# Kernel optimization log

Hardware: AMD Instinct MI355X
Metric: run time of the kernel (lower is better)

The kernel has to match this reference:

```python
import jax, jax.numpy as jnp
import numpy as np

G = 32        # group_num
PD = 8        # primary capsule dim
OC = 10       # output caps (classes)
OD = 16       # output dim
GS = 36       # group_size = primary spatial 6*6
N_ITERS = 3   # routing iterations


def conv2d(x, w, stride):
    return jax.lax.conv_general_dilated(
        x, w, window_strides=(stride, stride), padding='VALID',
        dimension_numbers=('NCHW', 'OIHW', 'NCHW'))


def squash(x):
    l2 = jnp.sum(x * x, axis=-1, keepdims=True)
    l = jnp.sqrt(l2)
    return x * (l2 / (1.0 + l2)) / (l + 1e-8)


def setup_inputs() -> dict:
    key = jax.random.key(0)
    ks = jax.random.split(key, 6)
    B = 256
    inp = jax.random.normal(ks[0], (B, 1, 28, 28), dtype=jnp.float32)
    W1 = jax.random.normal(ks[1], (256, 1, 9, 9), dtype=jnp.float32) * 0.05
    b1 = jnp.zeros((256,), dtype=jnp.float32)
    W2 = jax.random.normal(ks[2], (G * PD, 256, 9, 9), dtype=jnp.float32) * 0.01
    b2 = jnp.zeros((G * PD,), dtype=jnp.float32)
    Wcaps = jax.random.normal(ks[3], (G, GS, PD, OC * OD), dtype=jnp.float32) * 0.01
    b_route = jnp.zeros((G, 1, GS, OC), dtype=jnp.float32)
    return {'input': inp, 'W1': W1, 'b1': b1, 'W2': W2, 'b2': b2,
            'Wcaps': Wcaps, 'b_route': b_route}


def reference(input, W1, b1, W2, b2, Wcaps, b_route):
    B = input.shape[0]
    # conv1 + relu: (B,256,20,20)
    x = jax.nn.relu(conv2d(input, W1, 1) + b1[None, :, None, None])
    # primary caps conv: (B,256,6,6)
    y = conv2d(x, W2, 2) + b2[None, :, None, None]
    H = y.shape[2]
    # (B,G,PD,H,W) -> (B,G,H,W,PD) -> (B,G,GS,PD)
    y = y.reshape(B, G, PD, H, H).transpose(0, 1, 3, 4, 2).reshape(B, G, GS, PD)
    u = squash(y)
    # capsule predictions: (B,G,GS,OC,OD)
    up = jnp.einsum('bgsi,gsio->bgso', u, Wcaps).reshape(B, G, GS, OC, OD)
    # routing logits: (B,G,GS,OC)
    b = jnp.broadcast_to(jnp.transpose(b_route, (1, 0, 2, 3)), (B, G, GS, OC))
    v = None
    for r in range(N_ITERS):
        c = jax.nn.softmax(b, axis=3)                       # (B,G,GS,OC)
        s = jnp.einsum('bgso,bgsod->bgod', c, up)           # (B,G,OC,OD)
        v = squash(s)
        if r < N_ITERS - 1:
            b = b + jnp.einsum('bgsod,bgod->bgso', up, v)
    v = v.sum(axis=1)                                       # (B,OC,OD)
    probs = jnp.sqrt(jnp.sum(v * v, axis=2))                # (B,OC)
    return v, probs
```

## Files before the change

kernel.cpp:

```cpp
#include <hip/hip_runtime.h>
#include <math.h>


typedef float floatx4 __attribute__((ext_vector_type(4)));
typedef __bf16 bf16x8 __attribute__((ext_vector_type(8)));
typedef unsigned uintx4 __attribute__((ext_vector_type(4)));

#define XHI_OFF 0u
#define XLO_OFF 58720256u
#define WHI_OFF 117440512u
#define WLO_OFF 128974848u
#define Y2_OFF  140509184u
#define VP_OFF  0u
#define Y2_BYTES 9437184u

#define SL_IY   88
#define SL_IMG  1760
#define SL_PAR  7072
#define SL_STRIDE 14336

#define TAPSTRIDE 65536

__device__ __forceinline__ void bf16split(float v, short& hs, short& ls) {
  unsigned u = __builtin_bit_cast(unsigned, v);
  unsigned r = (u + 0x7FFFu + ((u >> 16) & 1u)) & 0xFFFF0000u;
  hs = (short)(r >> 16);
  float lo = v - __builtin_bit_cast(float, r);
  unsigned u2 = __builtin_bit_cast(unsigned, lo);
  unsigned r2 = u2 + 0x7FFFu + ((u2 >> 16) & 1u);
  ls = (short)(r2 >> 16);
}

__device__ __forceinline__ void stage7(const short* gp, short* lp) {
#pragma unroll
  for (int c = 0; c < 7; c++)
    __builtin_amdgcn_global_load_lds(
        (const __attribute__((address_space(1))) void*)(gp + c * 512),
        (__attribute__((address_space(3))) void*)(lp + c * 512), 16, 0, 0);
}

__global__ __launch_bounds__(320) void conv1_k(
    const float* __restrict__ inp, const float* __restrict__ W1,
    const float* __restrict__ b1, short* __restrict__ xhi,
    short* __restrict__ xlo) {
  __shared__ __align__(16) float img[784];
  __shared__ float wl[81 * 34];
  const int blk = blockIdx.x;
  const int b = blk >> 3;
  const int cbase = (blk & 7) * 32;
  const int t = threadIdx.x;

  const float4* src = (const float4*)(inp + b * 784);
  for (int idx = t; idx < 196; idx += 320) ((float4*)img)[idx] = src[idx];
  for (int idx = t; idx < 2592; idx += 320) {
    int c = idx / 81, tap = idx - c * 81;
    wl[tap * 34 + c] = W1[(cbase + c) * 81 + tap];
  }
  __syncthreads();

  const int oy = t >> 4;
  const int ct = t & 15;
  const int c0 = cbase + ct * 2;
  const float bias0 = b1[c0], bias1 = b1[c0 + 1];
  float acc0[20], acc1[20];
#pragma unroll
  for (int ox = 0; ox < 20; ox++) { acc0[ox] = bias0; acc1[ox] = bias1; }

#pragma unroll 1
  for (int i = 0; i < 9; i++) {
    float wr0[9], wr1[9];
#pragma unroll
    for (int j = 0; j < 9; j++) {
      float2 wv = *(const float2*)&wl[(i * 9 + j) * 34 + ct * 2];
      wr0[j] = wv.x; wr1[j] = wv.y;
    }
    float xr[28];
    const float4* rp = (const float4*)&img[(oy + i) * 28];
#pragma unroll
    for (int k = 0; k < 7; k++) {
      float4 v = rp[k];
      xr[4 * k] = v.x; xr[4 * k + 1] = v.y; xr[4 * k + 2] = v.z; xr[4 * k + 3] = v.w;
    }
#pragma unroll
    for (int j = 0; j < 9; j++)
#pragma unroll
      for (int ox = 0; ox < 20; ox++) {
        acc0[ox] = fmaf(xr[ox + j], wr0[j], acc0[ox]);
        acc1[ox] = fmaf(xr[ox + j], wr1[j], acc1[ox]);
      }
  }

  const int icgG = c0 >> 3;
  const long sbase = ((long)(icgG * 64 + (b >> 2))) * SL_STRIDE
                   + (long)(b & 3) * SL_IMG + (long)oy * SL_IY + (c0 & 7);
#pragma unroll
  for (int ox = 0; ox < 20; ox++) {
    float v0 = fmaxf(acc0[ox], 0.f), v1 = fmaxf(acc1[ox], 0.f);
    short h0, l0, h1, l1;
    bf16split(v0, h0, l0);
    bf16split(v1, h1, l1);
    long a = sbase + (ox & 1) * SL_PAR + (ox >> 1) * 8;
    *(short2*)&xhi[a] = make_short2(h0, h1);
    *(short2*)&xlo[a] = make_short2(l0, l1);
  }
  {
    long a0 = sbase + 80;
    *(short2*)&xhi[a0] = make_short2(0, 0);
    *(short2*)&xlo[a0] = make_short2(0, 0);
    long a1 = sbase + SL_PAR + 80;
    *(short2*)&xhi[a1] = make_short2(0, 0);
    *(short2*)&xlo[a1] = make_short2(0, 0);
  }
}

__global__ __launch_bounds__(256) void wtrans_k(
    const float* __restrict__ W2, short* __restrict__ whi,
    short* __restrict__ wlo) {
  __shared__ short lh[81 * 258];
  __shared__ short ll[81 * 258];
  const int blk = blockIdx.x;
  const int icg = blk & 31, ocg = blk >> 5;
  const int t = threadIdx.x;

  for (int idx = t; idx < 20736; idx += 256) {
    int c = idx / 648, r = idx - c * 648;
    int ics = r / 81, tap = r - ics * 81;
    float v = W2[(long)(ocg * 32 + c) * 20736 + icg * 648 + r];
    short h, l;
    bf16split(v, h, l);
    lh[tap * 258 + c * 8 + ics] = h;
    ll[tap * 258 + c * 8 + ics] = l;
  }
  __syncthreads();
  const long obase = (long)icg * 2048 + ocg * 256 + t;
#pragma unroll 1
  for (int tap = 0; tap < 88; tap++) {
    short h = 0, l = 0;
    if (tap < 81) { h = lh[tap * 258 + t]; l = ll[tap * 258 + t]; }
    whi[obase + (long)tap * TAPSTRIDE] = h;
    wlo[obase + (long)tap * TAPSTRIDE] = l;
  }
}

__global__ __launch_bounds__(256, 2) void conv2_k(
    const short* __restrict__ xhi, const short* __restrict__ xlo,
    const short* __restrict__ whi, const short* __restrict__ wlo,
    float* __restrict__ y2) {
  __shared__ __align__(16) short slab[2][SL_STRIDE];

  const int blk = blockIdx.x;
  const int ks = blk & 7;
  const int mb = blk >> 3;
  const int t = threadIdx.x;
  const int lane = t & 63;
  const int q = lane >> 4;
  const int ln16 = lane & 15;
  const int wv = t >> 6;

  int combo[9];
#pragma unroll
  for (int mt = 0; mt < 9; mt++) {
    int row = mt * 16 + ln16;
    int im = row / 36;
    int pos = row - im * 36;
    int oy = pos / 6, ox = pos - oy * 6;
    combo[mt] = im * SL_IMG + oy * (2 * SL_IY) + ox * 8;
  }

  floatx4 acc[9][4];
#pragma unroll
  for (int mt = 0; mt < 9; mt++)
#pragma unroll
    for (int nt = 0; nt < 4; nt++) acc[mt][nt] = (floatx4)0.f;

  const int stoff = wv * 7 * 512 + lane * 8;

  stage7(xhi + (long)(ks * 4 * 64 + mb) * SL_STRIDE + stoff, &slab[0][stoff]);

#pragma unroll 1
  for (int icg = 0; icg < 4; icg++) {
    const int icgG = ks * 4 + icg;
    const long wb0 = ((long)icgG * 256 + wv * 64 + ln16) * 8 + (long)q * TAPSTRIDE;

    __syncthreads();
    stage7(xlo + (long)(icgG * 64 + mb) * SL_STRIDE + stoff, &slab[1][stoff]);

    {
      bf16x8 cbh[4];
#pragma unroll
      for (int nt = 0; nt < 4; nt++) cbh[nt] = *(const bf16x8*)&whi[wb0 + nt * 128];
#pragma unroll 1
      for (int kst = 0; kst < 21; kst++) {
        const int t0n = (kst < 20) ? (kst + 1) * 4 : 80;
        bf16x8 nbh[4], cbl[4];
#pragma unroll
        for (int nt = 0; nt < 4; nt++) {
          nbh[nt] = *(const bf16x8*)&whi[wb0 + (long)t0n * TAPSTRIDE + nt * 128];
          cbl[nt] = *(const bf16x8*)&wlo[wb0 + (long)(kst * 4) * TAPSTRIDE + nt * 128];
        }
        const int tap = kst * 4 + q;
        const int i = tap / 9, j = tap - i * 9;
        const int aoff = (j & 1) * SL_PAR + i * SL_IY + (j >> 1) * 8;
#pragma unroll
        for (int bb = 0; bb < 3; bb++) {
          bf16x8 av[3];
#pragma unroll
          for (int m3 = 0; m3 < 3; m3++)
            av[m3] = *(const bf16x8*)&slab[0][aoff + combo[bb * 3 + m3]];
#pragma unroll
          for (int nt = 0; nt < 4; nt++)
#pragma unroll
            for (int m3 = 0; m3 < 3; m3++)
              acc[bb * 3 + m3][nt] = __builtin_amdgcn_mfma_f32_16x16x32_bf16(
                  av[m3], cbh[nt], acc[bb * 3 + m3][nt], 0, 0, 0);
#pragma unroll
          for (int nt = 0; nt < 4; nt++)
#pragma unroll
            for (int m3 = 0; m3 < 3; m3++)
              acc[bb * 3 + m3][nt] = __builtin_amdgcn_mfma_f32_16x16x32_bf16(
                  av[m3], cbl[nt], acc[bb * 3 + m3][nt], 0, 0, 0);
        }
#pragma unroll
        for (int nt = 0; nt < 4; nt++) cbh[nt] = nbh[nt];
      }
    }

    __syncthreads();
    if (icg < 3)
      stage7(xhi + (long)((icgG + 1) * 64 + mb) * SL_STRIDE + stoff, &slab[0][stoff]);

    {
      bf16x8 cbh[4];
#pragma unroll
      for (int nt = 0; nt < 4; nt++) cbh[nt] = *(const bf16x8*)&whi[wb0 + nt * 128];
#pragma unroll 1
      for (int kst = 0; kst < 21; kst++) {
        const int t0n = (kst < 20) ? (kst + 1) * 4 : 80;
        bf16x8 nbh[4];
#pragma unroll
        for (int nt = 0; nt < 4; nt++)
          nbh[nt] = *(const bf16x8*)&whi[wb0 + (long)t0n * TAPSTRIDE + nt * 128];
        const int tap = kst * 4 + q;
        const int i = tap / 9, j = tap - i * 9;
        const int aoff = (j & 1) * SL_PAR + i * SL_IY + (j >> 1) * 8;
#pragma unroll
        for (int bb = 0; bb < 3; bb++) {
          bf16x8 av[3];
#pragma unroll
          for (int m3 = 0; m3 < 3; m3++)
            av[m3] = *(const bf16x8*)&slab[1][aoff + combo[bb * 3 + m3]];
#pragma unroll
          for (int nt = 0; nt < 4; nt++)
#pragma unroll
            for (int m3 = 0; m3 < 3; m3++)
              acc[bb * 3 + m3][nt] = __builtin_amdgcn_mfma_f32_16x16x32_bf16(
                  av[m3], cbh[nt], acc[bb * 3 + m3][nt], 0, 0, 0);
        }
#pragma unroll
        for (int nt = 0; nt < 4; nt++) cbh[nt] = nbh[nt];
      }
    }
  }

#pragma unroll
  for (int mt = 0; mt < 9; mt++)
#pragma unroll
    for (int nt = 0; nt < 4; nt++) {
      int oc = wv * 64 + nt * 16 + ln16;
      int rowb = mb * 144 + mt * 16 + q * 4;
#pragma unroll
      for (int r = 0; r < 4; r++)
        atomicAdd(&y2[(long)(rowb + r) * 256 + oc], acc[mt][nt][r]);
    }
}

__global__ __launch_bounds__(256) void caps_k(
    const float* __restrict__ y2, const float* __restrict__ b2,
    const float* __restrict__ Wcaps, const float* __restrict__ b_route,
    float* __restrict__ vpart) {
  __shared__ float u[288];
  __shared__ float usc[36];
  __shared__ float up[5760];
  __shared__ float bl[360];
  __shared__ float cl[360];
  __shared__ float sv[160];
  __shared__ float vv[160];
  __shared__ float scale[10];
  const int blk = blockIdx.x;
  const int g = blk & 31, b = blk >> 5;
  const int t = threadIdx.x;

  for (int idx = t; idx < 288; idx += 256) {
    int s = idx >> 3, d = idx & 7;
    u[idx] = y2[((long)b * 36 + s) * 256 + g * 8 + d] + b2[g * 8 + d];
  }
  for (int idx = t; idx < 360; idx += 256) bl[idx] = b_route[g * 360 + idx];
  __syncthreads();
  if (t < 36) {
    float l2 = 0.f;
#pragma unroll
    for (int d = 0; d < 8; d++) { float v = u[t * 8 + d]; l2 = fmaf(v, v, l2); }
    float l = sqrtf(l2);
    usc[t] = (l2 / (1.f + l2)) / (l + 1e-8f);
  }
  __syncthreads();
  for (int idx = t; idx < 288; idx += 256) u[idx] *= usc[idx >> 3];
  __syncthreads();
  for (int idx = t; idx < 5760; idx += 256) {
    int s = idx / 160, k = idx - s * 160;
    const float* wp = Wcaps + (g * 36 + s) * 8 * 160 + k;
    float a = 0.f;
#pragma unroll
    for (int d = 0; d < 8; d++) a = fmaf(u[s * 8 + d], wp[d * 160], a);
    up[idx] = a;
  }
  __syncthreads();

  for (int r = 0; r < 3; r++) {
    if (t < 36) {
      float m = bl[t * 10];
#pragma unroll
      for (int oc = 1; oc < 10; oc++) m = fmaxf(m, bl[t * 10 + oc]);
      float e[10]; float sum = 0.f;
#pragma unroll
      for (int oc = 0; oc < 10; oc++) { e[oc] = expf(bl[t * 10 + oc] - m); sum += e[oc]; }
      float inv = 1.f / sum;
#pragma unroll
      for (int oc = 0; oc < 10; oc++) cl[t * 10 + oc] = e[oc] * inv;
    }
    __syncthreads();
    if (t < 160) {
      const int oc = t >> 4;
      float a = 0.f;
#pragma unroll 1
      for (int s = 0; s < 36; s++) a = fmaf(cl[s * 10 + oc], up[s * 160 + t], a);
      sv[t] = a;
    }
    __syncthreads();
    if (t < 10) {
      float l2 = 0.f;
#pragma unroll
      for (int od = 0; od < 16; od++) { float v = sv[t * 16 + od]; l2 = fmaf(v, v, l2); }
      scale[t] = (l2 / (1.f + l2)) / (sqrtf(l2) + 1e-8f);
    }
    __syncthreads();
    if (t < 160) vv[t] = sv[t] * scale[t >> 4];
    __syncthreads();
    if (r < 2) {
      for (int idx = t; idx < 360; idx += 256) {
        int s = idx / 10, oc = idx - s * 10;
        float a = 0.f;
#pragma unroll
        for (int od = 0; od < 16; od++)
          a = fmaf(up[s * 160 + oc * 16 + od], vv[oc * 16 + od], a);
        bl[idx] += a;
      }
      __syncthreads();
    }
  }
  if (t < 160) vpart[(b * 32 + g) * 160 + t] = vv[t];
}

__global__ __launch_bounds__(192) void final_k(
    const float* __restrict__ vpart, float* __restrict__ out) {
  __shared__ float v[160];
  const int b = blockIdx.x, t = threadIdx.x;
  if (t < 160) {
    float a = 0.f;
#pragma unroll 4
    for (int g = 0; g < 32; g++) a += vpart[(b * 32 + g) * 160 + t];
    v[t] = a;
    out[b * 160 + t] = a;
  }
  __syncthreads();
  if (t < 10) {
    float l2 = 0.f;
#pragma unroll
    for (int od = 0; od < 16; od++) { float x = v[t * 16 + od]; l2 = fmaf(x, x, l2); }
    out[40960 + b * 10 + t] = sqrtf(l2);
  }
}

extern "C" void kernel_launch(void* const* d_in, const int* in_sizes, int n_in,
                              void* d_out, int out_size, void* d_ws, size_t ws_size,
                              hipStream_t stream) {
  const float* inp     = (const float*)d_in[0];
  const float* W1      = (const float*)d_in[1];
  const float* b1      = (const float*)d_in[2];
  const float* W2      = (const float*)d_in[3];
  const float* b2      = (const float*)d_in[4];
  const float* Wcaps   = (const float*)d_in[5];
  const float* b_route = (const float*)d_in[6];
  float* out = (float*)d_out;
  char* ws = (char*)d_ws;

  short* xhi = (short*)(ws + XHI_OFF);
  short* xlo = (short*)(ws + XLO_OFF);
  short* whi = (short*)(ws + WHI_OFF);
  short* wlo = (short*)(ws + WLO_OFF);
  float* y2  = (float*)(ws + Y2_OFF);
  float* vp  = (float*)(ws + VP_OFF);

  (void)hipMemsetAsync(y2, 0, Y2_BYTES, stream);
  conv1_k <<<2048, 320, 0, stream>>>(inp, W1, b1, xhi, xlo);
  wtrans_k<<<256, 256, 0, stream>>>(W2, whi, wlo);
  conv2_k <<<512, 256, 0, stream>>>(xhi, xlo, whi, wlo, y2);
  caps_k  <<<8192, 256, 0, stream>>>(y2, b2, Wcaps, b_route, vp);
  final_k <<<256, 192, 0, stream>>>(vp, out);
}
```

Before: 520.9 us.

## Switch conv2 to 32x32x16 MFMA with 8-image slabs and 512-thread blocks

Conv2 now uses 32x32x16 bf16 MFMA tiles instead of 16x16x32. Each block handles 8 images (288 rows) with 8 waves of 32 output channels, in place of 4 images and 4 waves of 64 channels. The conv1 slab layout is doubled to match, and the grid is halved to 256 blocks of 512 threads. The aim is to cut B-operand reloads and raise MFMA efficiency per LDS read. In exchange the LDS footprint doubles, occupancy may drop, and per-iteration dependency chains get longer.

```diff
diff --git a/kernel.cpp b/kernel.cpp
--- a/kernel.cpp
+++ b/kernel.cpp
@@ -3,6 +3,7 @@
 
 
 typedef float floatx4 __attribute__((ext_vector_type(4)));
+typedef float floatx16 __attribute__((ext_vector_type(16)));
 typedef __bf16 bf16x8 __attribute__((ext_vector_type(8)));
 typedef unsigned uintx4 __attribute__((ext_vector_type(4)));
 
@@ -16,8 +17,8 @@
 
 #define SL_IY   88
 #define SL_IMG  1760
-#define SL_PAR  7072
-#define SL_STRIDE 14336
+#define SL_PAR  14144
+#define SL_STRIDE 28672
 
 #define TAPSTRIDE 65536
 
@@ -91,8 +92,8 @@
   }
 
   const int icgG = c0 >> 3;
-  const long sbase = ((long)(icgG * 64 + (b >> 2))) * SL_STRIDE
-                   + (long)(b & 3) * SL_IMG + (long)oy * SL_IY + (c0 & 7);
+  const long sbase = ((long)(icgG * 32 + (b >> 3))) * SL_STRIDE
+                   + (long)(b & 7) * SL_IMG + (long)oy * SL_IY + (c0 & 7);
 #pragma unroll
   for (int ox = 0; ox < 20; ox++) {
     float v0 = fmaxf(acc0[ox], 0.f), v1 = fmaxf(acc1[ox], 0.f);
@@ -142,7 +143,7 @@
   }
 }
 
-__global__ __launch_bounds__(256, 2) void conv2_k(
+__global__ __launch_bounds__(512, 2) void conv2_k(
     const short* __restrict__ xhi, const short* __restrict__ xlo,
     const short* __restrict__ whi, const short* __restrict__ wlo,
     float* __restrict__ y2) {
@@ -153,125 +154,93 @@
   const int mb = blk >> 3;
   const int t = threadIdx.x;
   const int lane = t & 63;
-  const int q = lane >> 4;
-  const int ln16 = lane & 15;
+  const int l31 = lane & 31;
+  const int h = lane >> 5;
   const int wv = t >> 6;
 
   int combo[9];
 #pragma unroll
   for (int mt = 0; mt < 9; mt++) {
-    int row = mt * 16 + ln16;
+    int row = mt * 32 + l31;
     int im = row / 36;
     int pos = row - im * 36;
     int oy = pos / 6, ox = pos - oy * 6;
     combo[mt] = im * SL_IMG + oy * (2 * SL_IY) + ox * 8;
   }
 
-  floatx4 acc[9][4];
-#pragma unroll
-  for (int mt = 0; mt < 9; mt++)
-#pragma unroll
-    for (int nt = 0; nt < 4; nt++) acc[mt][nt] = (floatx4)0.f;
+  floatx16 acc[9];
+#pragma unroll
+  for (int mt = 0; mt < 9; mt++) acc[mt] = (floatx16)0.f;
 
   const int stoff = wv * 7 * 512 + lane * 8;
 
-  stage7(xhi + (long)(ks * 4 * 64 + mb) * SL_STRIDE + stoff, &slab[0][stoff]);
+  stage7(xhi + (long)(ks * 4 * 32 + mb) * SL_STRIDE + stoff, &slab[0][stoff]);
 
 #pragma unroll 1
   for (int icg = 0; icg < 4; icg++) {
     const int icgG = ks * 4 + icg;
-    const long wb0 = ((long)icgG * 256 + wv * 64 + ln16) * 8 + (long)q * TAPSTRIDE;
-
-    __syncthreads();
-    stage7(xlo + (long)(icgG * 64 + mb) * SL_STRIDE + stoff, &slab[1][stoff]);
+    const long wb = (long)icgG * 2048 + (wv * 32 + l31) * 8 + (long)h * TAPSTRIDE;
+
+    __syncthreads();
+    stage7(xlo + (long)(icgG * 32 + mb) * SL_STRIDE + stoff, &slab[1][stoff]);
 
     {
-      bf16x8 cbh[4];
-#pragma unroll
-      for (int nt = 0; nt < 4; nt++) cbh[nt] = *(const bf16x8*)&whi[wb0 + nt * 128];
-#pragma unroll 1
-      for (int kst = 0; kst < 21; kst++) {
-        const int t0n = (kst < 20) ? (kst + 1) * 4 : 80;
-        bf16x8 nbh[4], cbl[4];
-#pragma unroll
-        for (int nt = 0; nt < 4; nt++) {
-          nbh[nt] = *(const bf16x8*)&whi[wb0 + (long)t0n * TAPSTRIDE + nt * 128];
-          cbl[nt] = *(const bf16x8*)&wlo[wb0 + (long)(kst * 4) * TAPSTRIDE + nt * 128];
-        }
-        const int tap = kst * 4 + q;
+      bf16x8 cbh = *(const bf16x8*)&whi[wb];
+#pragma unroll 1
+      for (int kst = 0; kst < 42; kst++) {
+        bf16x8 nbh = *(const bf16x8*)&whi[wb + (long)(2 * kst + 2) * TAPSTRIDE];
+        bf16x8 cbl = *(const bf16x8*)&wlo[wb + (long)(2 * kst) * TAPSTRIDE];
+        const int tap = 2 * kst + h;
         const int i = tap / 9, j = tap - i * 9;
         const int aoff = (j & 1) * SL_PAR + i * SL_IY + (j >> 1) * 8;
-#pragma unroll
-        for (int bb = 0; bb < 3; bb++) {
-          bf16x8 av[3];
-#pragma unroll
-          for (int m3 = 0; m3 < 3; m3++)
-            av[m3] = *(const bf16x8*)&slab[0][aoff + combo[bb * 3 + m3]];
-#pragma unroll
-          for (int nt = 0; nt < 4; nt++)
-#pragma unroll
-            for (int m3 = 0; m3 < 3; m3++)
-              acc[bb * 3 + m3][nt] = __builtin_amdgcn_mfma_f32_16x16x32_bf16(
-                  av[m3], cbh[nt], acc[bb * 3 + m3][nt], 0, 0, 0);
-#pragma unroll
-          for (int nt = 0; nt < 4; nt++)
-#pragma unroll
-            for (int m3 = 0; m3 < 3; m3++)
-              acc[bb * 3 + m3][nt] = __builtin_amdgcn_mfma_f32_16x16x32_bf16(
-                  av[m3], cbl[nt], acc[bb * 3 + m3][nt], 0, 0, 0);
-        }
-#pragma unroll
-        for (int nt = 0; nt < 4; nt++) cbh[nt] = nbh[nt];
+        bf16x8 av[9];
+#pragma unroll
+        for (int mt = 0; mt < 9; mt++)
+          av[mt] = *(const bf16x8*)&slab[0][aoff + combo[mt]];
+#pragma unroll
+        for (int mt = 0; mt < 9; mt++)
+          acc[mt] = __builtin_amdgcn_mfma_f32_32x32x16_bf16(av[mt], cbh, acc[mt], 0, 0, 0);
+#pragma unroll
+        for (int mt = 0; mt < 9; mt++)
+          acc[mt] = __builtin_amdgcn_mfma_f32_32x32x16_bf16(av[mt], cbl, acc[mt], 0, 0, 0);
+        cbh = nbh;
       }
     }
 
     __syncthreads();
     if (icg < 3)
-      stage7(xhi + (long)((icgG + 1) * 64 + mb) * SL_STRIDE + stoff, &slab[0][stoff]);
+      stage7(xhi + (long)((icgG + 1) * 32 + mb) * SL_STRIDE + stoff, &slab[0][stoff]);
 
     {
-      bf16x8 cbh[4];
-#pragma unroll
-      for (int nt = 0; nt < 4; nt++) cbh[nt] = *(const bf16x8*)&whi[wb0 + nt * 128];
-#pragma unroll 1
-      for (int kst = 0; kst < 21; kst++) {
-        const int t0n = (kst < 20) ? (kst + 1) * 4 : 80;
-        bf16x8 nbh[4];
-#pragma unroll
-        for (int nt = 0; nt < 4; nt++)
-          nbh[nt] = *(const bf16x8*)&whi[wb0 + (long)t0n * TAPSTRIDE + nt * 128];
-        const int tap = kst * 4 + q;
+      bf16x8 cbh = *(const bf16x8*)&whi[wb];
+#pragma unroll 1
+      for (int kst = 0; kst < 42; kst++) {
+        bf16x8 nbh = *(const bf16x8*)&whi[wb + (long)(2 * kst + 2) * TAPSTRIDE];
+        const int tap = 2 * kst + h;
         const int i = tap / 9, j = tap - i * 9;
         const int aoff = (j & 1) * SL_PAR + i * SL_IY + (j >> 1) * 8;
-#pragma unroll
-        for (int bb = 0; bb < 3; bb++) {
-          bf16x8 av[3];
-#pragma unroll
-          for (int m3 = 0; m3 < 3; m3++)
-            av[m3] = *(const bf16x8*)&slab[1][aoff + combo[bb * 3 + m3]];
-#pragma unroll
-          for (int nt = 0; nt < 4; nt++)
-#pragma unroll
-            for (int m3 = 0; m3 < 3; m3++)
-              acc[bb * 3 + m3][nt] = __builtin_amdgcn_mfma_f32_16x16x32_bf16(
-                  av[m3], cbh[nt], acc[bb * 3 + m3][nt], 0, 0, 0);
-        }
-#pragma unroll
-        for (int nt = 0; nt < 4; nt++) cbh[nt] = nbh[nt];
+        bf16x8 av[9];
+#pragma unroll
+        for (int mt = 0; mt < 9; mt++)
+          av[mt] = *(const bf16x8*)&slab[1][aoff + combo[mt]];
+#pragma unroll
+        for (int mt = 0; mt < 9; mt++)
+          acc[mt] = __builtin_amdgcn_mfma_f32_32x32x16_bf16(av[mt], cbh, acc[mt], 0, 0, 0);
+        cbh = nbh;
       }
     }
   }
 
-#pragma unroll
-  for (int mt = 0; mt < 9; mt++)
-#pragma unroll
-    for (int nt = 0; nt < 4; nt++) {
-      int oc = wv * 64 + nt * 16 + ln16;
-      int rowb = mb * 144 + mt * 16 + q * 4;
-#pragma unroll
-      for (int r = 0; r < 4; r++)
-        atomicAdd(&y2[(long)(rowb + r) * 256 + oc], acc[mt][nt][r]);
-    }
+  const int oc = wv * 32 + l31;
+#pragma unroll
+  for (int mt = 0; mt < 9; mt++) {
+    const int rowb = mb * 288 + mt * 32 + 4 * h;
+#pragma unroll
+    for (int r = 0; r < 16; r++) {
+      int row = rowb + (r & 3) + 8 * (r >> 2);
+      atomicAdd(&y2[(long)row * 256 + oc], acc[mt][r]);
+    }
+  }
 }
 
 __global__ __launch_bounds__(256) void caps_k(
@@ -404,7 +373,7 @@
   (void)hipMemsetAsync(y2, 0, Y2_BYTES, stream);
   conv1_k <<<2048, 320, 0, stream>>>(inp, W1, b1, xhi, xlo);
   wtrans_k<<<256, 256, 0, stream>>>(W2, whi, wlo);
-  conv2_k <<<512, 256, 0, stream>>>(xhi, xlo, whi, wlo, y2);
+  conv2_k <<<256, 512, 0, stream>>>(xhi, xlo, whi, wlo, y2);
   caps_k  <<<8192, 256, 0, stream>>>(y2, b2, Wcaps, b_route, vp);
   final_k <<<256, 192, 0, stream>>>(vp, out);
 }
```

Result: slower. 553.1 us (+6.2%).
